# Performance work log

Measured on AMD Instinct MI355X. Metric: run time of the kernel, lower is better.

Reference implementation:

```python
import jax, jax.numpy as jnp
import numpy as np

NX = 1024
LENGTH = 0.1
BATCH = 16
COF = 0.25 * (LENGTH / (NX - 1)) ** 2  # 0.25 * STRIDE^2 / TEMPER_COEFFICIENT


def setup_inputs() -> dict:
    key = jax.random.key(0)
    k1, k2 = jax.random.split(key)
    layout = jax.random.uniform(k1, (BATCH, NX, NX, 1), dtype=jnp.float32)
    heat = jax.random.normal(k2, (BATCH, NX, NX, 1), dtype=jnp.float32)
    return {"layout": layout, "heat": heat, "n_iter": 50}


def _stencil(x):
    # reflect-pad then 3x3 cross stencil: 0.25*(up+down+left+right), NHWC
    xp = jnp.pad(x, ((0, 0), (1, 1), (1, 1), (0, 0)), mode="reflect")
    return 0.25 * (
        xp[:, :-2, 1:-1, :] + xp[:, 2:, 1:-1, :]
        + xp[:, 1:-1, :-2, :] + xp[:, 1:-1, 2:, :]
    )


def reference(layout, heat, n_iter):
    f = COF * layout
    G = jnp.ones_like(heat)  # bcs=None -> no Dirichlet mask zeros

    def body(i, x):
        return G * (_stencil(x) + f)

    x0 = heat * G
    return jax.lax.fori_loop(0, n_iter, body, x0)
```

## Files before the change

### kernel.cpp

```cpp
#include <hip/hip_runtime.h>


#define NX 1024
#define BATCH 16
#define TSTEPS 10
#define OUT 44
#define HI 53
#define PITCH 64
#define LROWS 66

typedef float v2f __attribute__((ext_vector_type(2)));

__device__ __forceinline__ int reflect_idx(int i) {
    i = (i < 0) ? -i : i;
    return (i > NX - 1) ? 2 * (NX - 1) - i : i;
}

__device__ __forceinline__ float dpp_shr1(float x) {
    int v = __float_as_int(x);
    return __int_as_float(__builtin_amdgcn_update_dpp(v, v, 0x111, 0xF, 0xF, false));
}
__device__ __forceinline__ float dpp_shl1(float x) {
    int v = __float_as_int(x);
    return __int_as_float(__builtin_amdgcn_update_dpp(v, v, 0x101, 0xF, 0xF, false));
}

__device__ __forceinline__ v2f pk_add(v2f a, v2f b) {
    v2f d; asm("v_pk_add_f32 %0, %1, %2" : "=v"(d) : "v"(a), "v"(b)); return d;
}
__device__ __forceinline__ v2f pk_fma(v2f a, v2f b, v2f c) {
    v2f d; asm("v_pk_fma_f32 %0, %1, %2, %3" : "=v"(d) : "v"(a), "v"(b), "v"(c)); return d;
}

__global__ __launch_bounds__(256, 4) void jacobi_fused(const float* __restrict__ src,
                                                       const float* __restrict__ layout,
                                                       float* __restrict__ dst) {
    __shared__ float buf[2][LROWS * PITCH];

    const float COF = (float)(0.25 * (0.1 / 1023.0) * (0.1 / 1023.0));

    const int tid = threadIdx.x;
    const int g = tid & 15;
    const int c = tid >> 4;
    const int gr0 = blockIdx.y * OUT - TSTEPS;
    const int gc0 = blockIdx.x * OUT - TSTEPS;
    const int base = blockIdx.z * NX * NX;
    const int R0 = 1 + 4 * c;
    const int C0 = 4 * g;

    v2f fE[4], fO[4];

    const bool interior = (blockIdx.x >= 1) && (blockIdx.x <= 22) &&
                          (blockIdx.y >= 1) && (blockIdx.y <= 22);

    if (interior) {
        const float* sb = src + base + gr0 * NX + gc0;
#pragma unroll
        for (int k = 0; k < 8; ++k) {
            int idx2 = tid + 256 * k;
            int r = idx2 >> 5, q2 = idx2 & 31;
            v2f v = *(const v2f*)(sb + r * NX + 2 * q2);
            int lo = 4 * (q2 >> 1) + (q2 & 1);
            buf[0][r * PITCH + lo]     = v.x;
            buf[0][r * PITCH + lo + 2] = v.y;
        }
        const float* lb = layout + base + gc0 + C0;
#pragma unroll
        for (int i = 0; i < 4; ++i) {
            v2f a = *(const v2f*)(lb + (gr0 + R0 + i) * NX);
            v2f b = *(const v2f*)(lb + (gr0 + R0 + i) * NX + 2);
            fE[i] = (v2f){COF * a.x, COF * b.x};
            fO[i] = (v2f){COF * a.y, COF * b.y};
        }
    } else {
#pragma unroll
        for (int k = 0; k < 16; ++k) {
            int idx = tid + 256 * k;
            int r = idx >> 6, q = idx & 63;
            int lo = (q & ~3) | ((q & 1) << 1) | ((q >> 1) & 1);
            buf[0][r * PITCH + lo] = src[base + reflect_idx(gr0 + r) * NX + reflect_idx(gc0 + q)];
        }
#pragma unroll
        for (int i = 0; i < 4; ++i) {
            int grr = reflect_idx(gr0 + R0 + i);
            float f0 = layout[base + grr * NX + reflect_idx(gc0 + C0)];
            float f1 = layout[base + grr * NX + reflect_idx(gc0 + C0 + 1)];
            float f2 = layout[base + grr * NX + reflect_idx(gc0 + C0 + 2)];
            float f3 = layout[base + grr * NX + reflect_idx(gc0 + C0 + 3)];
            fE[i] = (v2f){COF * f0, COF * f2};
            fO[i] = (v2f){COF * f1, COF * f3};
        }
    }
    __syncthreads();

    v2f E[4], O[4];
#pragma unroll
    for (int i = 0; i < 4; ++i) {
        float4 v = *(const float4*)&buf[0][(R0 + i) * PITCH + C0];
        E[i] = (v2f){v.x, v.y};
        O[i] = (v2f){v.z, v.w};
    }

    const v2f qq = (v2f){0.25f, 0.25f};

#pragma unroll
    for (int s = 0; s < TSTEPS; ++s) {
        if (s > 0) {
            float* bb = buf[s & 1];
            *(float4*)&bb[R0 * PITCH + C0]       = make_float4(E[0].x, E[0].y, O[0].x, O[0].y);
            *(float4*)&bb[(R0 + 3) * PITCH + C0] = make_float4(E[3].x, E[3].y, O[3].x, O[3].y);
            __syncthreads();
        }
        const float* rb = (s == 0) ? buf[0] : buf[s & 1];
        float4 t  = *(const float4*)&rb[(R0 - 1) * PITCH + C0];
        float4 bo = *(const float4*)&rb[(R0 + 4) * PITCH + C0];
        v2f topE = (v2f){t.x, t.y},  topO = (v2f){t.z, t.w};
        v2f botE = (v2f){bo.x, bo.y}, botO = (v2f){bo.z, bo.w};

        v2f nE[4], nO[4];
#pragma unroll
        for (int i = 0; i < 4; ++i) {
            v2f upE = (i == 0) ? topE : E[i - 1], upO = (i == 0) ? topO : O[i - 1];
            v2f dnE = (i == 3) ? botE : E[i + 1], dnO = (i == 3) ? botO : O[i + 1];
            v2f vE = pk_add(upE, dnE);
            v2f vO = pk_add(upO, dnO);
            v2f P; P.x = dpp_shr1(O[i].y); P.y = O[i].x;
            v2f Q; Q.x = E[i].y; Q.y = dpp_shl1(E[i].x);
            v2f hE = pk_add(P, O[i]);
            v2f hO = pk_add(E[i], Q);
            nE[i] = pk_fma(pk_add(vE, hE), qq, fE[i]);
            nO[i] = pk_fma(pk_add(vO, hO), qq, fO[i]);
        }
#pragma unroll
        for (int i = 0; i < 4; ++i) { E[i] = nE[i]; O[i] = nO[i]; }
    }

#pragma unroll
    for (int i = 0; i < 4; ++i) {
        int br = R0 + i;
        bool rowok = (br >= TSTEPS) && (br <= HI) && (gr0 + br < NX);
        float v[4] = {E[i].x, O[i].x, E[i].y, O[i].y};
#pragma unroll
        for (int k = 0; k < 4; ++k) {
            int dcol = C0 + k;
            if (rowok && dcol >= TSTEPS && dcol <= HI && (gc0 + dcol) < NX)
                dst[base + (gr0 + br) * NX + (gc0 + dcol)] = v[k];
        }
    }
}

extern "C" void kernel_launch(void* const* d_in, const int* in_sizes, int n_in,
                              void* d_out, int out_size, void* d_ws, size_t ws_size,
                              hipStream_t stream) {
    const float* layout = (const float*)d_in[0];
    const float* heat   = (const float*)d_in[1];
    float* out = (float*)d_out;
    float* ws  = (float*)d_ws;

    dim3 grid((NX + OUT - 1) / OUT, (NX + OUT - 1) / OUT, BATCH);
    dim3 block(256);

    jacobi_fused<<<grid, block, 0, stream>>>(heat, layout, out);
    jacobi_fused<<<grid, block, 0, stream>>>(out,  layout, ws);
    jacobi_fused<<<grid, block, 0, stream>>>(ws,   layout, out);
    jacobi_fused<<<grid, block, 0, stream>>>(out,  layout, ws);
    jacobi_fused<<<grid, block, 0, stream>>>(ws,   layout, out);
}
```

Baseline: 451.6 us.

## Shrink LDS to halo-exchange slots and load tiles directly into registers

Each thread now loads its own 4x4 sub-tile of the source straight from global memory into registers, so the full 66-row tile is no longer staged through LDS. LDS keeps only per-thread-group halo slots (34 rows instead of 66) plus the two outer boundary rows, written by the first 128 threads. That cuts shared memory roughly in half, so launch bounds are raised to 8 blocks per SIMD to increase occupancy. The update loop is also done in place with a rolling 'up' register instead of separate next-state arrays, which lowers register pressure at the cost of one extra barrier in the first step.

```diff
diff --git a/kernel.cpp b/kernel.cpp
--- a/kernel.cpp
+++ b/kernel.cpp
@@ -7,7 +7,7 @@
 #define OUT 44
 #define HI 53
 #define PITCH 64
-#define LROWS 66
+#define SLOTS 34
 
 typedef float v2f __attribute__((ext_vector_type(2)));
 
@@ -32,10 +32,10 @@
     v2f d; asm("v_pk_fma_f32 %0, %1, %2, %3" : "=v"(d) : "v"(a), "v"(b), "v"(c)); return d;
 }
 
-__global__ __launch_bounds__(256, 4) void jacobi_fused(const float* __restrict__ src,
+__global__ __launch_bounds__(256, 8) void jacobi_fused(const float* __restrict__ src,
                                                        const float* __restrict__ layout,
                                                        float* __restrict__ dst) {
-    __shared__ float buf[2][LROWS * PITCH];
+    __shared__ float buf[2][SLOTS * PITCH];
 
     const float COF = (float)(0.25 * (0.1 / 1023.0) * (0.1 / 1023.0));
 
@@ -48,101 +48,104 @@
     const int R0 = 1 + 4 * c;
     const int C0 = 4 * g;
 
-    v2f fE[4], fO[4];
+    v2f E[4], O[4], fE[4], fO[4];
 
     const bool interior = (blockIdx.x >= 1) && (blockIdx.x <= 22) &&
                           (blockIdx.y >= 1) && (blockIdx.y <= 22);
 
     if (interior) {
-        const float* sb = src + base + gr0 * NX + gc0;
-#pragma unroll
-        for (int k = 0; k < 8; ++k) {
-            int idx2 = tid + 256 * k;
-            int r = idx2 >> 5, q2 = idx2 & 31;
-            v2f v = *(const v2f*)(sb + r * NX + 2 * q2);
-            int lo = 4 * (q2 >> 1) + (q2 & 1);
-            buf[0][r * PITCH + lo]     = v.x;
-            buf[0][r * PITCH + lo + 2] = v.y;
-        }
-        const float* lb = layout + base + gc0 + C0;
+        const float* sb = src + base + (gr0 + R0) * NX + gc0 + C0;
+        const float* lb = layout + base + (gr0 + R0) * NX + gc0 + C0;
 #pragma unroll
         for (int i = 0; i < 4; ++i) {
-            v2f a = *(const v2f*)(lb + (gr0 + R0 + i) * NX);
-            v2f b = *(const v2f*)(lb + (gr0 + R0 + i) * NX + 2);
+            v2f a = *(const v2f*)(sb + i * NX);
+            v2f b = *(const v2f*)(sb + i * NX + 2);
+            E[i] = (v2f){a.x, b.x};
+            O[i] = (v2f){a.y, b.y};
+        }
+#pragma unroll
+        for (int i = 0; i < 4; ++i) {
+            v2f a = *(const v2f*)(lb + i * NX);
+            v2f b = *(const v2f*)(lb + i * NX + 2);
             fE[i] = (v2f){COF * a.x, COF * b.x};
             fO[i] = (v2f){COF * a.y, COF * b.y};
         }
+        if (tid < 128) {
+            const int rsel = tid >> 6;
+            const int q2 = tid & 31;
+            const int slot = rsel ? 32 : 1;
+            v2f v = *(const v2f*)(src + base + (gr0 + (rsel ? 65 : 0)) * NX + gc0 + 2 * q2);
+            const int lo = 4 * (q2 >> 1) + (q2 & 1);
+            buf[0][slot * PITCH + lo]     = v.x;
+            buf[0][slot * PITCH + lo + 2] = v.y;
+        }
     } else {
 #pragma unroll
-        for (int k = 0; k < 16; ++k) {
-            int idx = tid + 256 * k;
-            int r = idx >> 6, q = idx & 63;
-            int lo = (q & ~3) | ((q & 1) << 1) | ((q >> 1) & 1);
-            buf[0][r * PITCH + lo] = src[base + reflect_idx(gr0 + r) * NX + reflect_idx(gc0 + q)];
+        for (int i = 0; i < 4; ++i) {
+            const int grr = reflect_idx(gr0 + R0 + i);
+            const float* sr = src + base + grr * NX;
+            const float* lr = layout + base + grr * NX;
+            const int c0 = reflect_idx(gc0 + C0);
+            const int c1 = reflect_idx(gc0 + C0 + 1);
+            const int c2 = reflect_idx(gc0 + C0 + 2);
+            const int c3 = reflect_idx(gc0 + C0 + 3);
+            E[i]  = (v2f){sr[c0], sr[c2]};
+            O[i]  = (v2f){sr[c1], sr[c3]};
+            fE[i] = (v2f){COF * lr[c0], COF * lr[c2]};
+            fO[i] = (v2f){COF * lr[c1], COF * lr[c3]};
         }
-#pragma unroll
-        for (int i = 0; i < 4; ++i) {
-            int grr = reflect_idx(gr0 + R0 + i);
-            float f0 = layout[base + grr * NX + reflect_idx(gc0 + C0)];
-            float f1 = layout[base + grr * NX + reflect_idx(gc0 + C0 + 1)];
-            float f2 = layout[base + grr * NX + reflect_idx(gc0 + C0 + 2)];
-            float f3 = layout[base + grr * NX + reflect_idx(gc0 + C0 + 3)];
-            fE[i] = (v2f){COF * f0, COF * f2};
-            fO[i] = (v2f){COF * f1, COF * f3};
+        if (tid < 128) {
+            const int rsel = tid >> 6;
+            const int q = tid & 63;
+            const int slot = rsel ? 32 : 1;
+            const int grr = reflect_idx(gr0 + (rsel ? 65 : 0));
+            const int lo = (q & ~3) | ((q & 1) << 1) | ((q >> 1) & 1);
+            buf[0][slot * PITCH + lo] = src[base + grr * NX + reflect_idx(gc0 + q)];
         }
-    }
-    __syncthreads();
-
-    v2f E[4], O[4];
-#pragma unroll
-    for (int i = 0; i < 4; ++i) {
-        float4 v = *(const float4*)&buf[0][(R0 + i) * PITCH + C0];
-        E[i] = (v2f){v.x, v.y};
-        O[i] = (v2f){v.z, v.w};
     }
 
     const v2f qq = (v2f){0.25f, 0.25f};
+    const int wT = (2 * c) * PITCH + C0;
+    const int wB = (2 * c + 3) * PITCH + C0;
+    const int rT = (2 * c + 1) * PITCH + C0;
+    const int rB = (2 * c + 2) * PITCH + C0;
 
 #pragma unroll
     for (int s = 0; s < TSTEPS; ++s) {
-        if (s > 0) {
-            float* bb = buf[s & 1];
-            *(float4*)&bb[R0 * PITCH + C0]       = make_float4(E[0].x, E[0].y, O[0].x, O[0].y);
-            *(float4*)&bb[(R0 + 3) * PITCH + C0] = make_float4(E[3].x, E[3].y, O[3].x, O[3].y);
-            __syncthreads();
-        }
-        const float* rb = (s == 0) ? buf[0] : buf[s & 1];
-        float4 t  = *(const float4*)&rb[(R0 - 1) * PITCH + C0];
-        float4 bo = *(const float4*)&rb[(R0 + 4) * PITCH + C0];
-        v2f topE = (v2f){t.x, t.y},  topO = (v2f){t.z, t.w};
-        v2f botE = (v2f){bo.x, bo.y}, botO = (v2f){bo.z, bo.w};
-
-        v2f nE[4], nO[4];
+        float* bb = buf[s & 1];
+        *(float4*)&bb[wT] = make_float4(E[0].x, E[0].y, O[0].x, O[0].y);
+        *(float4*)&bb[wB] = make_float4(E[3].x, E[3].y, O[3].x, O[3].y);
+        __syncthreads();
+        const float4 t  = *(const float4*)&bb[rT];
+        const float4 bo = *(const float4*)&bb[rB];
+        v2f upE = (v2f){t.x, t.y};
+        v2f upO = (v2f){t.z, t.w};
+        const v2f botE = (v2f){bo.x, bo.y};
+        const v2f botO = (v2f){bo.z, bo.w};
 #pragma unroll
         for (int i = 0; i < 4; ++i) {
-            v2f upE = (i == 0) ? topE : E[i - 1], upO = (i == 0) ? topO : O[i - 1];
-            v2f dnE = (i == 3) ? botE : E[i + 1], dnO = (i == 3) ? botO : O[i + 1];
+            v2f dnE = (i == 3) ? botE : E[i + 1];
+            v2f dnO = (i == 3) ? botO : O[i + 1];
             v2f vE = pk_add(upE, dnE);
             v2f vO = pk_add(upO, dnO);
             v2f P; P.x = dpp_shr1(O[i].y); P.y = O[i].x;
             v2f Q; Q.x = E[i].y; Q.y = dpp_shl1(E[i].x);
             v2f hE = pk_add(P, O[i]);
             v2f hO = pk_add(E[i], Q);
-            nE[i] = pk_fma(pk_add(vE, hE), qq, fE[i]);
-            nO[i] = pk_fma(pk_add(vO, hO), qq, fO[i]);
+            upE = E[i]; upO = O[i];
+            E[i] = pk_fma(pk_add(vE, hE), qq, fE[i]);
+            O[i] = pk_fma(pk_add(vO, hO), qq, fO[i]);
         }
-#pragma unroll
-        for (int i = 0; i < 4; ++i) { E[i] = nE[i]; O[i] = nO[i]; }
     }
 
 #pragma unroll
     for (int i = 0; i < 4; ++i) {
-        int br = R0 + i;
-        bool rowok = (br >= TSTEPS) && (br <= HI) && (gr0 + br < NX);
+        const int br = R0 + i;
+        const bool rowok = (br >= TSTEPS) && (br <= HI) && (gr0 + br < NX);
         float v[4] = {E[i].x, O[i].x, E[i].y, O[i].y};
 #pragma unroll
         for (int k = 0; k < 4; ++k) {
-            int dcol = C0 + k;
+            const int dcol = C0 + k;
             if (rowok && dcol >= TSTEPS && dcol <= HI && (gc0 + dcol) < NX)
                 dst[base + (gr0 + br) * NX + (gc0 + dcol)] = v[k];
         }
```

Result: no change. 459.9 us (+1.8%).
